# Optimization experiments

Hardware: AMD Instinct MI355X
Metric: run time of the kernel (lower is better)

Reference implementation:

```python
import jax, jax.numpy as jnp
import numpy as np

B, S, D, H = 2, 2048, 1024, 16
DK = D // H


def setup_inputs() -> dict:
    key = jax.random.key(0)
    ks = jax.random.split(key, 7)
    q = jax.random.normal(ks[0], (B, S, D), dtype=jnp.float32)
    k = jax.random.normal(ks[1], (B, S, D), dtype=jnp.float32)
    v = jax.random.normal(ks[2], (B, S, D), dtype=jnp.float32)
    # causal mask: mask==0 positions get -1e9 before softmax
    mask = jnp.tril(jnp.ones((S, S), dtype=jnp.int32))[None, None, :, :]
    scale = 0.02
    w_q = jax.random.normal(ks[3], (D, D), dtype=jnp.float32) * scale
    w_k = jax.random.normal(ks[4], (D, D), dtype=jnp.float32) * scale
    w_v = jax.random.normal(ks[5], (D, D), dtype=jnp.float32) * scale
    w_o = jax.random.normal(ks[6], (D, D), dtype=jnp.float32) * scale
    return {"q": q, "k": k, "v": v, "mask": mask,
            "w_q": w_q, "w_k": w_k, "w_v": w_v, "w_o": w_o}


def reference(q, k, v, mask, w_q, w_k, w_v, w_o):
    # nn.Linear(bias=False): x @ W.T
    query = q @ w_q.T  # [B,S,D]
    key = k @ w_k.T
    value = v @ w_v.T
    # split heads -> [B,H,S,DK]
    query = query.reshape(B, S, H, DK).transpose(0, 2, 1, 3)
    key = key.reshape(B, S, H, DK).transpose(0, 2, 1, 3)
    value = value.reshape(B, S, H, DK).transpose(0, 2, 1, 3)
    scores = jnp.einsum('bhqd,bhkd->bhqk', query, key) / jnp.sqrt(
        jnp.asarray(DK, dtype=query.dtype))
    scores = jnp.where(mask == 0, jnp.asarray(-1e9, scores.dtype), scores)
    attn = jax.nn.softmax(scores, axis=-1)  # dropout p=0.0 -> identity
    x = jnp.einsum('bhqk,bhkd->bhqd', attn, value)  # [B,H,S,DK]
    x = x.transpose(0, 2, 1, 3).reshape(B, S, D)
    return x @ w_o.T
```

## Files before the change

kernel.cpp:

```cpp
#include <hip/hip_runtime.h>

typedef __attribute__((ext_vector_type(8))) short short8;
typedef __attribute__((ext_vector_type(4))) float f32x4;

#define DEVI static __device__ __forceinline__

constexpr int BB = 2, SS = 2048, DD = 1024, HH = 16, DKK = 64;
constexpr size_t QN = (size_t)BB * SS * DD;
constexpr size_t WN = (size_t)DD * DD;

constexpr size_t OFF_WQ = 3 * QN;
constexpr size_t OFF_WO = OFF_WQ + 3 * WN;
constexpr size_t OFF_QM = OFF_WQ + 4 * WN;
constexpr size_t OFF_KM = OFF_QM + QN;
constexpr size_t OFF_VM = OFF_QM + 2 * QN;
constexpr size_t OFF_XC = OFF_QM + 3 * QN;

DEVI unsigned short f2bf(float f) {
  unsigned int u = __float_as_uint(f);
  u = (u + 0x7fffu + ((u >> 16) & 1u)) >> 16;
  return (unsigned short)u;
}

DEVI f32x4 fzero() { f32x4 z = {0.f, 0.f, 0.f, 0.f}; return z; }

DEVI void gld16(const void* g, void* l) {
  __builtin_amdgcn_global_load_lds((__attribute__((address_space(1))) void*)g,
                                   (__attribute__((address_space(3))) void*)l,
                                   16, 0, 0);
}

DEVI short8 mk8u(unsigned int a, unsigned int b, unsigned int c, unsigned int d) {
  union { short8 s; unsigned int u[4]; } x;
  x.u[0] = a; x.u[1] = b; x.u[2] = c; x.u[3] = d;
  return x.s;
}

DEVI short8 mk8q(unsigned long long lo, unsigned long long hi) {
  union { short8 s; unsigned long long q[2]; } x;
  x.q[0] = lo; x.q[1] = hi;
  return x.s;
}

DEVI unsigned int pkbf(float a, float b) {
  return __builtin_amdgcn_perm(__float_as_uint(b), __float_as_uint(a), 0x07060302u);
}

__global__ __launch_bounds__(256) void convert_all(
    const float* __restrict__ q, const float* __restrict__ k,
    const float* __restrict__ v, const float* __restrict__ wq,
    const float* __restrict__ wk, const float* __restrict__ wv,
    const float* __restrict__ wo, unsigned short* __restrict__ ws) {
  size_t t = (size_t)blockIdx.x * 256 + threadIdx.x;
  size_t e = t * 4;
  const float* src;
  size_t base, idx;
  if (e < 3 * QN) {
    size_t a = e >> 22;
    idx = e & (QN - 1);
    src = (a == 0) ? q : (a == 1) ? k : v;
    base = a * QN;
  } else {
    size_t r = e - 3 * QN;
    size_t a = r >> 20;
    idx = r & (WN - 1);
    src = (a == 0) ? wq : (a == 1) ? wk : (a == 2) ? wv : wo;
    base = 3 * QN + a * WN;
  }
  float4 f = *(const float4*)(src + idx);
  ushort4 o;
  o.x = f2bf(f.x); o.y = f2bf(f.y); o.z = f2bf(f.z); o.w = f2bf(f.w);
  *(ushort4*)(ws + base + idx) = o;
}

DEVI void gemm_tile_sb(const unsigned short* __restrict__ A,
                       const unsigned short* __restrict__ Bw,
                       unsigned short* ldsA, unsigned short* ldsB,
                       int m0, int n0, f32x4 acc[4][4]) {
  const int tid = threadIdx.x;
  const int w = tid >> 6, l = tid & 63;
  const int lr = l & 15, qd = l >> 4;
  const int wr = w >> 1, wc = w & 1;

#pragma unroll
  for (int i = 0; i < 4; ++i)
#pragma unroll
    for (int j = 0; j < 4; ++j) acc[i][j] = fzero();

  const unsigned short* pa[4];
  const unsigned short* pb[4];
  int ls[4];
#pragma unroll
  for (int u = 0; u < 4; ++u) {
    int s = w * 4 + u;
    int t16 = s >> 1, kt = s & 1;
    pa[u] = A + (size_t)(m0 + t16 * 16 + lr) * DD + kt * 32 + qd * 8;
    pb[u] = Bw + (size_t)(n0 + t16 * 16 + lr) * DD + kt * 32 + qd * 8;
    ls[u] = s * 512;
  }

#pragma unroll
  for (int u = 0; u < 4; ++u) gld16(pa[u], ldsA + ls[u]);
#pragma unroll
  for (int u = 0; u < 4; ++u) gld16(pb[u], ldsB + ls[u]);

  constexpr int NIT = DD / 64;
#pragma unroll 1
  for (int it = 0; it < NIT; ++it) {
    __syncthreads();
#pragma unroll
    for (int ks = 0; ks < 2; ++ks) {
      short8 af[4], bf[4];
#pragma unroll
      for (int im = 0; im < 4; ++im)
        af[im] = *(const short8*)&ldsA[((wr * 4 + im) * 2 + ks) * 512 + l * 8];
#pragma unroll
      for (int in = 0; in < 4; ++in)
        bf[in] = *(const short8*)&ldsB[((wc * 4 + in) * 2 + ks) * 512 + l * 8];
#pragma unroll
      for (int im = 0; im < 4; ++im)
#pragma unroll
        for (int in = 0; in < 4; ++in)
          acc[im][in] = __builtin_amdgcn_mfma_f32_16x16x32_bf16(
              af[im], bf[in], acc[im][in], 0, 0, 0);
    }
    if (it + 1 < NIT) {
      __syncthreads();
      const int k1 = (it + 1) * 64;
#pragma unroll
      for (int u = 0; u < 4; ++u) gld16(pa[u] + k1, ldsA + ls[u]);
#pragma unroll
      for (int u = 0; u < 4; ++u) gld16(pb[u] + k1, ldsB + ls[u]);
    }
  }
}

DEVI void gemm64_db(const unsigned short* __restrict__ A,
                    const unsigned short* __restrict__ Bw,
                    unsigned short* ldsA, unsigned short* ldsB,
                    int m0, int n0, f32x4 acc[4][2]) {
  const int tid = threadIdx.x;
  const int w = tid >> 6, l = tid & 63;
  const int lr = l & 15, qd = l >> 4;

#pragma unroll
  for (int i = 0; i < 4; ++i)
#pragma unroll
    for (int j = 0; j < 2; ++j) acc[i][j] = fzero();

  const unsigned short* pa[2];
  const unsigned short* pb[4];
  int lsa[2], lsb[4];
#pragma unroll
  for (int kh = 0; kh < 2; ++kh) {
    pa[kh] = A + (size_t)(m0 + w * 16 + lr) * DD + kh * 32 + qd * 8;
    lsa[kh] = (w * 2 + kh) * 512;
  }
#pragma unroll
  for (int r = 0; r < 2; ++r)
#pragma unroll
    for (int kh = 0; kh < 2; ++kh) {
      pb[r * 2 + kh] = Bw + (size_t)(n0 + (2 * w + r) * 16 + lr) * DD + kh * 32 + qd * 8;
      lsb[r * 2 + kh] = ((2 * w + r) * 2 + kh) * 512;
    }

#pragma unroll
  for (int u = 0; u < 2; ++u) gld16(pa[u], ldsA + lsa[u]);
#pragma unroll
  for (int u = 0; u < 4; ++u) gld16(pb[u], ldsB + lsb[u]);

  constexpr int NIT = DD / 64;
#pragma unroll 1
  for (int it = 0; it < NIT; ++it) {
    __syncthreads();
    const int curA = (it & 1) * 4096, curB = (it & 1) * 8192;
    if (it + 1 < NIT) {
      const int k1 = (it + 1) * 64;
      const int nxtA = 4096 - curA, nxtB = 8192 - curB;
#pragma unroll
      for (int u = 0; u < 2; ++u) gld16(pa[u] + k1, ldsA + nxtA + lsa[u]);
#pragma unroll
      for (int u = 0; u < 4; ++u) gld16(pb[u] + k1, ldsB + nxtB + lsb[u]);
    }
#pragma unroll
    for (int ks = 0; ks < 2; ++ks) {
      short8 af[4], bf[2];
#pragma unroll
      for (int im = 0; im < 4; ++im)
        af[im] = *(const short8*)&ldsA[curA + (im * 2 + ks) * 512 + l * 8];
#pragma unroll
      for (int in = 0; in < 2; ++in)
        bf[in] = *(const short8*)&ldsB[curB + ((2 * w + in) * 2 + ks) * 512 + l * 8];
#pragma unroll
      for (int im = 0; im < 4; ++im)
#pragma unroll
        for (int in = 0; in < 2; ++in)
          acc[im][in] = __builtin_amdgcn_mfma_f32_16x16x32_bf16(
              af[im], bf[in], acc[im][in], 0, 0, 0);
    }
  }
}

__global__ __launch_bounds__(256) void proj_gemm(unsigned short* __restrict__ ws) {
  __shared__ unsigned short ldsA[8192];
  __shared__ unsigned short ldsB[8192];
  const int z = blockIdx.z;
  const unsigned short* A = ws + (size_t)z * QN;
  const unsigned short* W = ws + OFF_WQ + (size_t)z * WN;
  unsigned short* O = ws + OFF_QM + (size_t)z * QN;
  const int m0 = blockIdx.x * 128, n0 = blockIdx.y * 128;
  f32x4 acc[4][4];
  gemm_tile_sb(A, W, ldsA, ldsB, m0, n0, acc);

  const int tid = threadIdx.x;
  const int w = tid >> 6, l = tid & 63, lr = l & 15, qd = l >> 4;
  const int wr = w >> 1, wc = w & 1;
  if (z == 2) {
#pragma unroll
    for (int im = 0; im < 4; ++im)
#pragma unroll
      for (int in = 0; in < 4; ++in) {
        const int n = n0 + wc * 64 + in * 16 + lr;
        const int h = n >> 6, dk = n & 63;
        const int m = m0 + wr * 64 + im * 16 + qd * 4;
        const int b = m >> 11, s = m & 2047;
        ushort4 pk;
        pk.x = f2bf(acc[im][in][0]); pk.y = f2bf(acc[im][in][1]);
        pk.z = f2bf(acc[im][in][2]); pk.w = f2bf(acc[im][in][3]);
        *(ushort4*)&O[((size_t)(b * HH + h) * DKK + dk) * SS + s] = pk;
      }
  } else {
#pragma unroll
    for (int im = 0; im < 4; ++im)
#pragma unroll
      for (int in = 0; in < 4; ++in) {
        const int n = n0 + wc * 64 + in * 16 + lr;
        const int h = n >> 6, dk = n & 63;
#pragma unroll
        for (int i = 0; i < 4; ++i) {
          const int m = m0 + wr * 64 + im * 16 + qd * 4 + i;
          const int b = m >> 11, s = m & 2047;
          O[((size_t)(b * HH + h) * SS + s) * DKK + dk] = f2bf(acc[im][in][i]);
        }
      }
  }
}

__global__ __launch_bounds__(512) void flash_attn(
    const unsigned short* __restrict__ Qm, const unsigned short* __restrict__ Km,
    const unsigned short* __restrict__ Vt, unsigned short* __restrict__ Xc) {
  __shared__ unsigned short Kl[2][4096];
  __shared__ unsigned short Vl[2][4096];
  const int p = blockIdx.x, head = blockIdx.y, b = blockIdx.z;
  const int tid = threadIdx.x, w = tid >> 6, l = tid & 63, lr = l & 15, qd = l >> 4;
  const size_t bh = (size_t)(b * HH + head);
  const unsigned short* Qb = Qm + bh * SS * DKK;
  const unsigned short* Kb = Km + bh * SS * DKK;
  const unsigned short* Vb = Vt + bh * DKK * SS;

  const bool heavy = (w < 4);
  const int qt = heavy ? (31 - p) : p;
  const int nkv = 32 - p;
  const int qrow = qt * 64 + (w & 3) * 16 + lr;

  const int s0 = heavy ? w : (w - 4);
  const int s1 = s0 + 4;
  const int loOff = ((qd >> 1) * 16 + lr) * 8 + (qd & 1) * 4;
  const int hiOff = ((2 + (qd >> 1)) * 16 + lr) * 8 + (qd & 1) * 4;

  short8 qf0 = *(const short8*)&Qb[(size_t)qrow * DKK + qd * 8];
  short8 qf1 = *(const short8*)&Qb[(size_t)qrow * DKK + 32 + qd * 8];

  f32x4 o[4];
#pragma unroll
  for (int i = 0; i < 4; ++i) o[i] = fzero();
  float ll = 0.f;
  const float c1 = 0.18033688011112042f;
  const float mc = 8.0f * c1;

  {
    if (heavy) {
      gld16(&Kb[(size_t)((s0 >> 1) * 16 + lr) * DKK + (s0 & 1) * 32 + qd * 8],
            &Kl[0][s0 * 512]);
      gld16(&Kb[(size_t)((s1 >> 1) * 16 + lr) * DKK + (s1 & 1) * 32 + qd * 8],
            &Kl[0][s1 * 512]);
    } else {
      gld16(&Vb[(size_t)((s0 >> 1) * 16 + lr) * SS + (s0 & 1) * 32 + qd * 8],
            &Vl[0][s0 * 512]);
      gld16(&Vb[(size_t)((s1 >> 1) * 16 + lr) * SS + (s1 & 1) * 32 + qd * 8],
            &Vl[0][s1 * 512]);
    }
  }

#pragma unroll 1
  for (int kv = 0; kv < nkv; ++kv) {
    __syncthreads();
    const int cur = kv & 1;
    if (kv + 1 < nkv) {
      const int kv0n = (kv + 1) * 64;
      if (heavy) {
        gld16(&Kb[(size_t)(kv0n + (s0 >> 1) * 16 + lr) * DKK + (s0 & 1) * 32 + qd * 8],
              &Kl[cur ^ 1][s0 * 512]);
        gld16(&Kb[(size_t)(kv0n + (s1 >> 1) * 16 + lr) * DKK + (s1 & 1) * 32 + qd * 8],
              &Kl[cur ^ 1][s1 * 512]);
      } else {
        gld16(&Vb[(size_t)((s0 >> 1) * 16 + lr) * SS + kv0n + (s0 & 1) * 32 + qd * 8],
              &Vl[cur ^ 1][s0 * 512]);
        gld16(&Vb[(size_t)((s1 >> 1) * 16 + lr) * SS + kv0n + (s1 & 1) * 32 + qd * 8],
              &Vl[cur ^ 1][s1 * 512]);
      }
    }

    if (kv <= qt) {
      const int kv0 = kv * 64;
      f32x4 sc[4];
#pragma unroll
      for (int nt = 0; nt < 4; ++nt) {
        short8 kf0 = *(const short8*)&Kl[cur][(nt * 2 + 0) * 512 + l * 8];
        short8 kf1 = *(const short8*)&Kl[cur][(nt * 2 + 1) * 512 + l * 8];
        f32x4 zz = fzero();
        zz = __builtin_amdgcn_mfma_f32_16x16x32_bf16(kf0, qf0, zz, 0, 0, 0);
        sc[nt] = __builtin_amdgcn_mfma_f32_16x16x32_bf16(kf1, qf1, zz, 0, 0, 0);
      }
      if (kv == qt) {
#pragma unroll
        for (int nt = 0; nt < 4; ++nt)
#pragma unroll
          for (int i = 0; i < 4; ++i) {
            const int kvi = kv0 + nt * 16 + qd * 4 + i;
            if (kvi > qrow) sc[nt][i] = -3e38f;
          }
      }

      float rs = 0.f;
#pragma unroll
      for (int nt = 0; nt < 4; ++nt)
#pragma unroll
        for (int i = 0; i < 4; ++i) {
          const float pp = exp2f(fmaf(sc[nt][i], c1, -mc));
          sc[nt][i] = pp;
          rs += pp;
        }
      rs += __shfl_xor(rs, 16);
      rs += __shfl_xor(rs, 32);
      ll += rs;

      unsigned int pd[4][2];
#pragma unroll
      for (int f = 0; f < 4; ++f) {
        pd[f][0] = pkbf(sc[f][0], sc[f][1]);
        pd[f][1] = pkbf(sc[f][2], sc[f][3]);
      }

#pragma unroll
      for (int kh = 0; kh < 2; ++kh) {
        short8 bfr = mk8u(pd[2 * kh][0], pd[2 * kh][1],
                          pd[2 * kh + 1][0], pd[2 * kh + 1][1]);
#pragma unroll
        for (int mt = 0; mt < 4; ++mt) {
          const int sbase = (mt * 2 + kh) * 512;
          const unsigned long long lo =
              *(const unsigned long long*)&Vl[cur][sbase + loOff];
          const unsigned long long hi =
              *(const unsigned long long*)&Vl[cur][sbase + hiOff];
          o[mt] = __builtin_amdgcn_mfma_f32_16x16x32_bf16(mk8q(lo, hi), bfr,
                                                          o[mt], 0, 0, 0);
        }
      }
    }
  }

  const float inv = 1.0f / ll;
  unsigned short* Xr = Xc + ((size_t)b * SS + qrow) * DD + (size_t)head * DKK;
#pragma unroll
  for (int mt = 0; mt < 4; ++mt)
#pragma unroll
    for (int i = 0; i < 4; ++i)
      Xr[mt * 16 + qd * 4 + i] = f2bf(o[mt][i] * inv);
}

__global__ __launch_bounds__(256) void out_gemm(
    const unsigned short* __restrict__ Xc, const unsigned short* __restrict__ Wo,
    float* __restrict__ out) {
  __shared__ unsigned short ldsA[8192];
  __shared__ unsigned short ldsB[16384];
  const int m0 = blockIdx.x * 64, n0 = blockIdx.y * 128;
  f32x4 acc[4][2];
  gemm64_db(Xc, Wo, ldsA, ldsB, m0, n0, acc);

  const int tid = threadIdx.x;
  const int w = tid >> 6, l = tid & 63, lr = l & 15, qd = l >> 4;
#pragma unroll
  for (int im = 0; im < 4; ++im)
#pragma unroll
    for (int in = 0; in < 2; ++in) {
      const int n = n0 + w * 32 + in * 16 + lr;
#pragma unroll
      for (int i = 0; i < 4; ++i) {
        const int m = m0 + im * 16 + qd * 4 + i;
        out[(size_t)m * DD + n] = acc[im][in][i];
      }
    }
}

extern "C" void kernel_launch(void* const* d_in, const int* in_sizes, int n_in,
                              void* d_out, int out_size, void* d_ws, size_t ws_size,
                              hipStream_t stream) {
  (void)in_sizes; (void)n_in; (void)out_size; (void)ws_size;
  const float* q  = (const float*)d_in[0];
  const float* k  = (const float*)d_in[1];
  const float* v  = (const float*)d_in[2];
  const float* wq = (const float*)d_in[4];
  const float* wk = (const float*)d_in[5];
  const float* wv = (const float*)d_in[6];
  const float* wo = (const float*)d_in[7];
  unsigned short* ws = (unsigned short*)d_ws;
  float* out = (float*)d_out;

  convert_all<<<dim3(16384), dim3(256), 0, stream>>>(q, k, v, wq, wk, wv, wo, ws);
  proj_gemm<<<dim3(32, 8, 3), dim3(256), 0, stream>>>(ws);
  flash_attn<<<dim3(16, 16, 2), dim3(512), 0, stream>>>(ws + OFF_QM, ws + OFF_KM,
                                                        ws + OFF_VM, ws + OFF_XC);
  out_gemm<<<dim3(64, 8), dim3(256), 0, stream>>>(ws + OFF_XC, ws + OFF_WO, out);
}
```

Before: 253.7 us.

## Triple-buffer LDS in projection GEMM with prefetch two K-steps ahead

Replaces the single-buffered projection GEMM mainloop, which had two barriers per 64-wide K step, with a triple-buffered pipeline over 32-wide K steps. Each step waits with a partial vmcnt plus a barrier, then issues the global-to-LDS loads for step t+2 before computing on step t. This is meant to hide global load latency behind MFMA work and remove one barrier per iteration. In exchange, LDS use per block grows and the loop runs twice as many iterations, each with less work.

```diff
diff --git a/kernel.cpp b/kernel.cpp
--- a/kernel.cpp
+++ b/kernel.cpp
@@ -73,7 +73,7 @@
   *(ushort4*)(ws + base + idx) = o;
 }
 
-DEVI void gemm_tile_sb(const unsigned short* __restrict__ A,
+DEVI void gemm_tile_tb(const unsigned short* __restrict__ A,
                        const unsigned short* __restrict__ Bw,
                        unsigned short* ldsA, unsigned short* ldsB,
                        int m0, int n0, f32x4 acc[4][4]) {
@@ -87,51 +87,61 @@
 #pragma unroll
     for (int j = 0; j < 4; ++j) acc[i][j] = fzero();
 
-  const unsigned short* pa[4];
-  const unsigned short* pb[4];
-  int ls[4];
-#pragma unroll
-  for (int u = 0; u < 4; ++u) {
-    int s = w * 4 + u;
-    int t16 = s >> 1, kt = s & 1;
-    pa[u] = A + (size_t)(m0 + t16 * 16 + lr) * DD + kt * 32 + qd * 8;
-    pb[u] = Bw + (size_t)(n0 + t16 * 16 + lr) * DD + kt * 32 + qd * 8;
+  const unsigned short* pa[2];
+  const unsigned short* pb[2];
+  int ls[2];
+#pragma unroll
+  for (int u = 0; u < 2; ++u) {
+    const int s = w * 2 + u;
+    pa[u] = A + (size_t)(m0 + s * 16 + lr) * DD + qd * 8;
+    pb[u] = Bw + (size_t)(n0 + s * 16 + lr) * DD + qd * 8;
     ls[u] = s * 512;
   }
 
-#pragma unroll
-  for (int u = 0; u < 4; ++u) gld16(pa[u], ldsA + ls[u]);
-#pragma unroll
-  for (int u = 0; u < 4; ++u) gld16(pb[u], ldsB + ls[u]);
-
-  constexpr int NIT = DD / 64;
+  constexpr int NIT = DD / 32;
+  constexpr int BUFSZ = 4096;
+
+#pragma unroll
+  for (int u = 0; u < 2; ++u) gld16(pa[u], ldsA + 0 * BUFSZ + ls[u]);
+#pragma unroll
+  for (int u = 0; u < 2; ++u) gld16(pb[u], ldsB + 0 * BUFSZ + ls[u]);
+#pragma unroll
+  for (int u = 0; u < 2; ++u) gld16(pa[u] + 32, ldsA + 1 * BUFSZ + ls[u]);
+#pragma unroll
+  for (int u = 0; u < 2; ++u) gld16(pb[u] + 32, ldsB + 1 * BUFSZ + ls[u]);
+
+  int rb = 0;
+  int wb = 2;
 #pragma unroll 1
-  for (int it = 0; it < NIT; ++it) {
-    __syncthreads();
-#pragma unroll
-    for (int ks = 0; ks < 2; ++ks) {
-      short8 af[4], bf[4];
-#pragma unroll
-      for (int im = 0; im < 4; ++im)
-        af[im] = *(const short8*)&ldsA[((wr * 4 + im) * 2 + ks) * 512 + l * 8];
+  for (int t = 0; t < NIT; ++t) {
+    if (t == NIT - 1) {
+      asm volatile("s_waitcnt vmcnt(0)\n\ts_barrier" ::: "memory");
+    } else {
+      asm volatile("s_waitcnt vmcnt(4)\n\ts_barrier" ::: "memory");
+    }
+    if (t + 2 < NIT) {
+      const int k2 = (t + 2) * 32;
+#pragma unroll
+      for (int u = 0; u < 2; ++u) gld16(pa[u] + k2, ldsA + wb * BUFSZ + ls[u]);
+#pragma unroll
+      for (int u = 0; u < 2; ++u) gld16(pb[u] + k2, ldsB + wb * BUFSZ + ls[u]);
+    }
+    const int rbase = rb * BUFSZ;
+    short8 af[4], bf[4];
+#pragma unroll
+    for (int im = 0; im < 4; ++im)
+      af[im] = *(const short8*)&ldsA[rbase + (wr * 4 + im) * 512 + l * 8];
+#pragma unroll
+    for (int in = 0; in < 4; ++in)
+      bf[in] = *(const short8*)&ldsB[rbase + (wc * 4 + in) * 512 + l * 8];
+#pragma unroll
+    for (int im = 0; im < 4; ++im)
 #pragma unroll
       for (int in = 0; in < 4; ++in)
-        bf[in] = *(const short8*)&ldsB[((wc * 4 + in) * 2 + ks) * 512 + l * 8];
-#pragma unroll
-      for (int im = 0; im < 4; ++im)
-#pragma unroll
-        for (int in = 0; in < 4; ++in)
-          acc[im][in] = __builtin_amdgcn_mfma_f32_16x16x32_bf16(
-              af[im], bf[in], acc[im][in], 0, 0, 0);
-    }
-    if (it + 1 < NIT) {
-      __syncthreads();
-      const int k1 = (it + 1) * 64;
-#pragma unroll
-      for (int u = 0; u < 4; ++u) gld16(pa[u] + k1, ldsA + ls[u]);
-#pragma unroll
-      for (int u = 0; u < 4; ++u) gld16(pb[u] + k1, ldsB + ls[u]);
-    }
+        acc[im][in] = __builtin_amdgcn_mfma_f32_16x16x32_bf16(
+            af[im], bf[in], acc[im][in], 0, 0, 0);
+    rb = (rb == 2) ? 0 : rb + 1;
+    wb = (wb == 2) ? 0 : wb + 1;
   }
 }
 
@@ -202,15 +212,15 @@
 }
 
 __global__ __launch_bounds__(256) void proj_gemm(unsigned short* __restrict__ ws) {
-  __shared__ unsigned short ldsA[8192];
-  __shared__ unsigned short ldsB[8192];
+  __shared__ unsigned short ldsA[12288];
+  __shared__ unsigned short ldsB[12288];
   const int z = blockIdx.z;
   const unsigned short* A = ws + (size_t)z * QN;
   const unsigned short* W = ws + OFF_WQ + (size_t)z * WN;
   unsigned short* O = ws + OFF_QM + (size_t)z * QN;
   const int m0 = blockIdx.x * 128, n0 = blockIdx.y * 128;
   f32x4 acc[4][4];
-  gemm_tile_sb(A, W, ldsA, ldsB, m0, n0, acc);
+  gemm_tile_tb(A, W, ldsA, ldsB, m0, n0, acc);
 
   const int tid = threadIdx.x;
   const int w = tid >> 6, l = tid & 63, lr = l & 15, qd = l >> 4;
```

Measured after the change: 257.1 us. About the same (+1.3%).

## Rewrite QKV projection GEMM with 256x256 tiles, double-buffered swizzled LDS

Applied to the files above, without the earlier changes.

Replaces the 128x128 single-buffered projection GEMM with a 512-thread, 256x256-tile kernel. It double-buffers 64 KB of LDS with an XOR-swizzled layout and issues the next tile's loads in quarters interleaved with the MFMA phases, using explicit vmcnt and barrier waits. It also raises wave priority around the MFMAs and remaps block indices into a 1D grid of 192 blocks to group tiles for cache locality. The aim is more operand reuse, fewer LDS bank conflicts, and hiding global load latency behind compute, at the cost of fewer blocks (192 on the GPU's CUs) and heavy register use for the 128 accumulators.

```diff
diff --git a/kernel.cpp b/kernel.cpp
--- a/kernel.cpp
+++ b/kernel.cpp
@@ -45,6 +45,13 @@
 DEVI unsigned int pkbf(float a, float b) {
   return __builtin_amdgcn_perm(__float_as_uint(b), __float_as_uint(a), 0x07060302u);
 }
+
+#define VMBAR(N) asm volatile("s_waitcnt vmcnt(" #N ")\n\ts_barrier" ::: "memory")
+#define LGKM0                                      \
+  do {                                             \
+    asm volatile("s_waitcnt lgkmcnt(0)" ::: "memory"); \
+    __builtin_amdgcn_sched_barrier(0);             \
+  } while (0)
 
 __global__ __launch_bounds__(256) void convert_all(
     const float* __restrict__ q, const float* __restrict__ k,
@@ -73,65 +80,160 @@
   *(ushort4*)(ws + base + idx) = o;
 }
 
-DEVI void gemm_tile_sb(const unsigned short* __restrict__ A,
-                       const unsigned short* __restrict__ Bw,
-                       unsigned short* ldsA, unsigned short* ldsB,
-                       int m0, int n0, f32x4 acc[4][4]) {
+__global__ __launch_bounds__(512, 2) void proj_gemm(unsigned short* __restrict__ ws) {
+  __shared__ unsigned short lds[65536];
   const int tid = threadIdx.x;
   const int w = tid >> 6, l = tid & 63;
-  const int lr = l & 15, qd = l >> 4;
-  const int wr = w >> 1, wc = w & 1;
-
-#pragma unroll
-  for (int i = 0; i < 4; ++i)
+  const int lr = l & 15, qd = l >> 4, l7 = l & 7, l3 = l >> 3;
+  const int wr = w >> 2, wc = w & 3;
+
+  const int orig = blockIdx.x;
+  const int swz = (orig & 7) * 24 + (orig >> 3);
+  const int mt = swz >> 2, nt = swz & 3;
+  const int z = mt >> 4;
+  const int m0 = (mt & 15) * 256, n0 = nt * 256;
+
+  const unsigned short* Ab = ws + (size_t)z * QN;
+  const unsigned short* Wb = ws + OFF_WQ + (size_t)z * WN;
+  unsigned short* O = ws + OFF_QM + (size_t)z * QN;
+
+  f32x4 acc[8][4];
+#pragma unroll
+  for (int i = 0; i < 8; ++i)
 #pragma unroll
     for (int j = 0; j < 4; ++j) acc[i][j] = fzero();
 
-  const unsigned short* pa[4];
-  const unsigned short* pb[4];
-  int ls[4];
-#pragma unroll
-  for (int u = 0; u < 4; ++u) {
-    int s = w * 4 + u;
-    int t16 = s >> 1, kt = s & 1;
-    pa[u] = A + (size_t)(m0 + t16 * 16 + lr) * DD + kt * 32 + qd * 8;
-    pb[u] = Bw + (size_t)(n0 + t16 * 16 + lr) * DD + kt * 32 + qd * 8;
-    ls[u] = s * 512;
-  }
-
-#pragma unroll
-  for (int u = 0; u < 4; ++u) gld16(pa[u], ldsA + ls[u]);
-#pragma unroll
-  for (int u = 0; u < 4; ++u) gld16(pb[u], ldsB + ls[u]);
-
-  constexpr int NIT = DD / 64;
+  auto stage = [&](int buf, int ab, int h, int kt) {
+    const unsigned short* src = ab ? Wb : Ab;
+    const int rc0 = (ab ? n0 : m0) + h * 128 + w * 8 + l3;
+    const int kofs = kt * 64 + ((l7 ^ l3) * 8);
+    unsigned short* d = &lds[buf * 32768 + ab * 16384 + h * 8192 + w * 512];
+#pragma unroll
+    for (int u = 0; u < 2; ++u)
+      gld16(src + (size_t)(rc0 + u * 64) * DD + kofs, d + u * 4096);
+  };
+  auto rdA = [&](int buf, int fi, int ks) -> short8 {
+    const int rg = (fi * 2 + wr) * 16 + lr;
+    const int c2 = (ks * 4 + qd) ^ l7;
+    return *(const short8*)&lds[buf * 32768 + rg * 64 + c2 * 8];
+  };
+  auto rdB = [&](int buf, int fj, int ks) -> short8 {
+    const int rg = (fj * 4 + wc) * 16 + lr;
+    const int c2 = (ks * 4 + qd) ^ l7;
+    return *(const short8*)&lds[buf * 32768 + 16384 + rg * 64 + c2 * 8];
+  };
+
+  stage(0, 0, 0, 0);
+  stage(0, 1, 0, 0);
+  stage(0, 1, 1, 0);
+  stage(0, 0, 1, 0);
+
+  constexpr int NT = DD / 64;
 #pragma unroll 1
-  for (int it = 0; it < NIT; ++it) {
-    __syncthreads();
-#pragma unroll
-    for (int ks = 0; ks < 2; ++ks) {
-      short8 af[4], bf[4];
-#pragma unroll
-      for (int im = 0; im < 4; ++im)
-        af[im] = *(const short8*)&ldsA[((wr * 4 + im) * 2 + ks) * 512 + l * 8];
-#pragma unroll
-      for (int in = 0; in < 4; ++in)
-        bf[in] = *(const short8*)&ldsB[((wc * 4 + in) * 2 + ks) * 512 + l * 8];
-#pragma unroll
-      for (int im = 0; im < 4; ++im)
-#pragma unroll
-        for (int in = 0; in < 4; ++in)
-          acc[im][in] = __builtin_amdgcn_mfma_f32_16x16x32_bf16(
-              af[im], bf[in], acc[im][in], 0, 0, 0);
-    }
-    if (it + 1 < NIT) {
-      __syncthreads();
-      const int k1 = (it + 1) * 64;
-#pragma unroll
-      for (int u = 0; u < 4; ++u) gld16(pa[u] + k1, ldsA + ls[u]);
-#pragma unroll
-      for (int u = 0; u < 4; ++u) gld16(pb[u] + k1, ldsB + ls[u]);
-    }
+  for (int t = 0; t < NT; ++t) {
+    const int rb = t & 1, wb = rb ^ 1;
+    const bool g = (t + 1 < NT);
+    short8 af[4][2], bf[2][2], bh[2][2];
+
+    VMBAR(4);
+    if (g) stage(wb, 0, 0, t + 1);
+#pragma unroll
+    for (int mi = 0; mi < 4; ++mi)
+#pragma unroll
+      for (int ks = 0; ks < 2; ++ks) af[mi][ks] = rdA(rb, mi, ks);
+#pragma unroll
+    for (int nj = 0; nj < 2; ++nj)
+#pragma unroll
+      for (int ks = 0; ks < 2; ++ks) bf[nj][ks] = rdB(rb, nj, ks);
+    LGKM0;
+    __builtin_amdgcn_s_setprio(1);
+#pragma unroll
+    for (int mi = 0; mi < 4; ++mi)
+#pragma unroll
+      for (int nj = 0; nj < 2; ++nj)
+#pragma unroll
+        for (int ks = 0; ks < 2; ++ks)
+          acc[mi][nj] = __builtin_amdgcn_mfma_f32_16x16x32_bf16(
+              af[mi][ks], bf[nj][ks], acc[mi][nj], 0, 0, 0);
+    __builtin_amdgcn_s_setprio(0);
+
+    if (g) { VMBAR(4); } else { VMBAR(2); }
+    if (g) stage(wb, 1, 0, t + 1);
+#pragma unroll
+    for (int nj = 0; nj < 2; ++nj)
+#pragma unroll
+      for (int ks = 0; ks < 2; ++ks) bh[nj][ks] = rdB(rb, 2 + nj, ks);
+    LGKM0;
+    __builtin_amdgcn_s_setprio(1);
+#pragma unroll
+    for (int mi = 0; mi < 4; ++mi)
+#pragma unroll
+      for (int nj = 0; nj < 2; ++nj)
+#pragma unroll
+        for (int ks = 0; ks < 2; ++ks)
+          acc[mi][2 + nj] = __builtin_amdgcn_mfma_f32_16x16x32_bf16(
+              af[mi][ks], bh[nj][ks], acc[mi][2 + nj], 0, 0, 0);
+    __builtin_amdgcn_s_setprio(0);
+
+    if (g) { VMBAR(4); } else { VMBAR(0); }
+    if (g) stage(wb, 1, 1, t + 1);
+#pragma unroll
+    for (int mi = 0; mi < 4; ++mi)
+#pragma unroll
+      for (int ks = 0; ks < 2; ++ks) af[mi][ks] = rdA(rb, 4 + mi, ks);
+    LGKM0;
+    __builtin_amdgcn_s_setprio(1);
+#pragma unroll
+    for (int mi = 0; mi < 4; ++mi)
+#pragma unroll
+      for (int nj = 0; nj < 2; ++nj)
+#pragma unroll
+        for (int ks = 0; ks < 2; ++ks)
+          acc[4 + mi][nj] = __builtin_amdgcn_mfma_f32_16x16x32_bf16(
+              af[mi][ks], bf[nj][ks], acc[4 + mi][nj], 0, 0, 0);
+    __builtin_amdgcn_s_setprio(0);
+
+    if (g) stage(wb, 0, 1, t + 1);
+    __builtin_amdgcn_s_setprio(1);
+#pragma unroll
+    for (int mi = 0; mi < 4; ++mi)
+#pragma unroll
+      for (int nj = 0; nj < 2; ++nj)
+#pragma unroll
+        for (int ks = 0; ks < 2; ++ks)
+          acc[4 + mi][2 + nj] = __builtin_amdgcn_mfma_f32_16x16x32_bf16(
+              af[mi][ks], bh[nj][ks], acc[4 + mi][2 + nj], 0, 0, 0);
+    __builtin_amdgcn_s_setprio(0);
+  }
+
+  if (z == 2) {
+#pragma unroll
+    for (int fi = 0; fi < 8; ++fi)
+#pragma unroll
+      for (int fj = 0; fj < 4; ++fj) {
+        const int n = n0 + (fj * 4 + wc) * 16 + lr;
+        const int h = n >> 6, dk = n & 63;
+        const int m = m0 + (fi * 2 + wr) * 16 + qd * 4;
+        const int b = m >> 11, s = m & 2047;
+        ushort4 pk;
+        pk.x = f2bf(acc[fi][fj][0]); pk.y = f2bf(acc[fi][fj][1]);
+        pk.z = f2bf(acc[fi][fj][2]); pk.w = f2bf(acc[fi][fj][3]);
+        *(ushort4*)&O[((size_t)(b * HH + h) * DKK + dk) * SS + s] = pk;
+      }
+  } else {
+#pragma unroll
+    for (int fi = 0; fi < 8; ++fi)
+#pragma unroll
+      for (int fj = 0; fj < 4; ++fj) {
+        const int n = n0 + (fj * 4 + wc) * 16 + lr;
+        const int h = n >> 6, dk = n & 63;
+#pragma unroll
+        for (int i = 0; i < 4; ++i) {
+          const int m = m0 + (fi * 2 + wr) * 16 + qd * 4 + i;
+          const int b = m >> 11, s = m & 2047;
+          O[((size_t)(b * HH + h) * SS + s) * DKK + dk] = f2bf(acc[fi][fj][i]);
+        }
+      }
   }
 }
 
@@ -198,51 +300,6 @@
           acc[im][in] = __builtin_amdgcn_mfma_f32_16x16x32_bf16(
               af[im], bf[in], acc[im][in], 0, 0, 0);
     }
-  }
-}
-
-__global__ __launch_bounds__(256) void proj_gemm(unsigned short* __restrict__ ws) {
-  __shared__ unsigned short ldsA[8192];
-  __shared__ unsigned short ldsB[8192];
-  const int z = blockIdx.z;
-  const unsigned short* A = ws + (size_t)z * QN;
-  const unsigned short* W = ws + OFF_WQ + (size_t)z * WN;
-  unsigned short* O = ws + OFF_QM + (size_t)z * QN;
-  const int m0 = blockIdx.x * 128, n0 = blockIdx.y * 128;
-  f32x4 acc[4][4];
-  gemm_tile_sb(A, W, ldsA, ldsB, m0, n0, acc);
-
-  const int tid = threadIdx.x;
-  const int w = tid >> 6, l = tid & 63, lr = l & 15, qd = l >> 4;
-  const int wr = w >> 1, wc = w & 1;
-  if (z == 2) {
-#pragma unroll
-    for (int im = 0; im < 4; ++im)
-#pragma unroll
-      for (int in = 0; in < 4; ++in) {
-        const int n = n0 + wc * 64 + in * 16 + lr;
-        const int h = n >> 6, dk = n & 63;
-        const int m = m0 + wr * 64 + im * 16 + qd * 4;
-        const int b = m >> 11, s = m & 2047;
-        ushort4 pk;
-        pk.x = f2bf(acc[im][in][0]); pk.y = f2bf(acc[im][in][1]);
-        pk.z = f2bf(acc[im][in][2]); pk.w = f2bf(acc[im][in][3]);
-        *(ushort4*)&O[((size_t)(b * HH + h) * DKK + dk) * SS + s] = pk;
-      }
-  } else {
-#pragma unroll
-    for (int im = 0; im < 4; ++im)
-#pragma unroll
-      for (int in = 0; in < 4; ++in) {
-        const int n = n0 + wc * 64 + in * 16 + lr;
-        const int h = n >> 6, dk = n & 63;
-#pragma unroll
-        for (int i = 0; i < 4; ++i) {
-          const int m = m0 + wr * 64 + im * 16 + qd * 4 + i;
-          const int b = m >> 11, s = m & 2047;
-          O[((size_t)(b * HH + h) * SS + s) * DKK + dk] = f2bf(acc[im][in][i]);
-        }
-      }
   }
 }
 
@@ -418,7 +475,7 @@
   float* out = (float*)d_out;
 
   convert_all<<<dim3(16384), dim3(256), 0, stream>>>(q, k, v, wq, wk, wv, wo, ws);
-  proj_gemm<<<dim3(32, 8, 3), dim3(256), 0, stream>>>(ws);
+  proj_gemm<<<dim3(192), dim3(512), 0, stream>>>(ws);
   flash_attn<<<dim3(16, 16, 2), dim3(512), 0, stream>>>(ws + OFF_QM, ws + OFF_KM,
                                                         ws + OFF_VM, ws + OFF_XC);
   out_gemm<<<dim3(64, 8), dim3(256), 0, stream>>>(ws + OFF_XC, ws + OFF_WO, out);
```

Measured after the change: 229.3 us. 9.6% less time.
